# Optimization experiments

Hardware: AMD Instinct MI355X
Metric: run time of the kernel (lower is better)

Reference implementation:

```python
import jax, jax.numpy as jnp
import numpy as np

N_HEADS = 16
LOCAL_WINDOW = 512
MAX_REL_DIST = 128
NEG_INF = jnp.float32(-1e30)


def setup_inputs() -> dict:
    key = jax.random.key(0)
    ks = jax.random.split(key, 5)
    B, T, C = 2, 2048, 1024
    x = jax.random.normal(ks[0], (B, T, C), dtype=jnp.float32)
    w_qkv = jax.random.normal(ks[1], (3 * C, C), dtype=jnp.float32) * 0.02
    w_proj = jax.random.normal(ks[2], (C, C), dtype=jnp.float32) * 0.02
    b_proj = jax.random.normal(ks[3], (C,), dtype=jnp.float32) * 0.02
    rel_bias = jax.random.normal(ks[4], (2 * MAX_REL_DIST + 1, N_HEADS), dtype=jnp.float32) * 0.02
    return {"x": x, "w_qkv": w_qkv, "w_proj": w_proj, "b_proj": b_proj, "rel_bias": rel_bias}


def reference(x, w_qkv, w_proj, b_proj, rel_bias):
    B, T, C = x.shape
    H = N_HEADS
    hd = C // H
    scale = hd ** -0.5
    # qkv projection: (B,T,3C) -> (3,B,H,T,hd)
    qkv = (x @ w_qkv.T).reshape(B, T, 3, H, hd).transpose(2, 0, 3, 1, 4)
    q, k, v = qkv[0], qkv[1], qkv[2]
    # full TxT scores (faithful to eager original)
    attn = jnp.einsum('bhqd,bhkd->bhqk', q, k) * scale
    i = jnp.arange(T)[:, None]
    j = jnp.arange(T)[None, :]
    mask = (i >= j) & (jnp.abs(i - j) <= LOCAL_WINDOW)
    attn = jnp.where(mask[None, None], attn, NEG_INF)
    # relative position bias: (H,T,T)
    rel = jnp.clip(i - j, -MAX_REL_DIST, MAX_REL_DIST) + MAX_REL_DIST
    bias = rel_bias[rel].transpose(2, 0, 1)  # (H,T,T)
    attn = attn + bias[None]
    attn = jax.nn.softmax(attn, axis=-1)
    y = jnp.einsum('bhqk,bhkd->bhqd', attn, v)
    y = y.transpose(0, 2, 1, 3).reshape(B, T, C)
    y = y @ w_proj.T + b_proj
    return y
```

## Files before the change

kernel.cpp:

```cpp
#include <hip/hip_runtime.h>

#define T_SEQ 2048
#define HD 64

typedef float f32x4 __attribute__((ext_vector_type(4)));
typedef __bf16 bf16x8 __attribute__((ext_vector_type(8)));
typedef unsigned short ushort4v __attribute__((ext_vector_type(4)));
typedef unsigned short ushort8v __attribute__((ext_vector_type(8)));

__device__ __forceinline__ unsigned short f2bf(float f) {
    unsigned u = __builtin_bit_cast(unsigned, f);
    u += 0x7fffu + ((u >> 16) & 1u);
    return (unsigned short)(u >> 16);
}

__device__ __forceinline__ void gll16(const void* g, void* lds) {
    __builtin_amdgcn_global_load_lds(
        (const __attribute__((address_space(1))) unsigned int*)g,
        (__attribute__((address_space(3))) unsigned int*)lds, 16, 0, 0);
}

__device__ __forceinline__ bf16x8 ldfrag(const unsigned short* p) {
    return __builtin_bit_cast(bf16x8, *reinterpret_cast<const ushort8v*>(p));
}

__global__ __launch_bounds__(256)
void cvt_all_kernel(const float* __restrict__ x, const float* __restrict__ wq,
                    const float* __restrict__ wp, unsigned short* __restrict__ xb,
                    unsigned short* __restrict__ wqb, unsigned short* __restrict__ wpb)
{
    int bid = blockIdx.x;
    const float* s; unsigned short* d; int off;
    if (bid < 2048)      { s = x;  d = xb;  off = bid; }
    else if (bid < 3584) { s = wq; d = wqb; off = bid - 2048; }
    else                 { s = wp; d = wpb; off = bid - 3584; }
    int i = (off * 256 + threadIdx.x) * 8;
    f32x4 a = *reinterpret_cast<const f32x4*>(s + i);
    f32x4 b = *reinterpret_cast<const f32x4*>(s + i + 4);
    ushort8v o;
#pragma unroll
    for (int j = 0; j < 4; ++j) { o[j] = f2bf(a[j]); o[4 + j] = f2bf(b[j]); }
    *reinterpret_cast<ushort8v*>(d + i) = o;
}

__global__ __launch_bounds__(512, 6)
void gemm_qkv_kernel(const unsigned short* __restrict__ A, const unsigned short* __restrict__ W,
                     unsigned short* __restrict__ qo, unsigned short* __restrict__ ko,
                     unsigned short* __restrict__ vo)
{
    constexpr int K = 1024;
    __shared__ unsigned short As[128 * 32];
    __shared__ unsigned short Bs[128 * 32];
    const int t = threadIdx.x;
    const int m0 = blockIdx.x * 128, n0 = blockIdx.y * 128;
    const int lane = t & 63, w = t >> 6;
    const int wy = w >> 1, wx = w & 1;
    const int l15 = lane & 15, quad = lane >> 4;

    f32x4 acc[2][4] = {};
    const char* Ab = (const char*)A;
    const char* Wb = (const char*)W;

    const int srow = w * 16 + (lane >> 2);
    const int slot = (lane & 3) ^ ((lane >> 2) & 3);

    for (int kcl = 0; kcl < K; kcl += 32) {
        gll16(Ab + ((size_t)(n0 + srow) * K + kcl + slot * 8) * 2, (char*)As + w * 1024);
        gll16(Wb + ((size_t)(m0 + srow) * K + kcl + slot * 8) * 2, (char*)Bs + w * 1024);
        __syncthreads();
        bf16x8 af[2], bfr[4];
#pragma unroll
        for (int nt = 0; nt < 2; ++nt)
            af[nt] = ldfrag(As + (wy * 32 + nt * 16 + l15) * 32 + ((quad ^ (l15 & 3)) * 8));
#pragma unroll
        for (int mt = 0; mt < 4; ++mt)
            bfr[mt] = ldfrag(Bs + (wx * 64 + mt * 16 + l15) * 32 + ((quad ^ (l15 & 3)) * 8));
#pragma unroll
        for (int nt = 0; nt < 2; ++nt)
#pragma unroll
            for (int mt = 0; mt < 4; ++mt)
                acc[nt][mt] = __builtin_amdgcn_mfma_f32_16x16x32_bf16(af[nt], bfr[mt], acc[nt][mt], 0, 0, 0);
        __syncthreads();
    }

    const int s = m0 >> 10;
#pragma unroll
    for (int nt = 0; nt < 2; ++nt) {
#pragma unroll
        for (int mt = 0; mt < 4; ++mt) {
            const int m = m0 + wx * 64 + mt * 16 + l15;
            const int h = (m >> 6) & 15, d = m & 63;
#pragma unroll
            for (int r = 0; r < 4; ++r) {
                const int n = n0 + wy * 32 + nt * 16 + quad * 4 + r;
                const int bb = n >> 11, tt = n & 2047;
                float val = acc[nt][mt][r];
                if (s == 0)
                    qo[((size_t)((bb << 4) + h) * T_SEQ + tt) * HD + d] = f2bf(val * 0.125f);
                else if (s == 1)
                    ko[((size_t)((bb << 4) + h) * T_SEQ + tt) * HD + d] = f2bf(val);
                else
                    vo[((size_t)((bb << 4) + h) * HD + d) * T_SEQ + tt] = f2bf(val);
            }
        }
    }
}

__global__ __launch_bounds__(256)
void gemm_proj_kernel(const unsigned short* __restrict__ A, const unsigned short* __restrict__ W,
                      float* __restrict__ o0, const float* __restrict__ bias)
{
    constexpr int K = 1024;
    __shared__ unsigned short As[64 * 32];
    __shared__ unsigned short Bs[64 * 32];
    const int t = threadIdx.x;
    const int m0 = blockIdx.x * 64, n0 = blockIdx.y * 64;
    const int lane = t & 63, w = t >> 6;
    const int wy = w >> 1, wx = w & 1;
    const int l15 = lane & 15, quad = lane >> 4;

    f32x4 acc[2][2] = {};
    const char* Ab = (const char*)A;
    const char* Wb = (const char*)W;
    const int srow = t >> 2;
    const int skc = (t & 3) ^ (srow & 3);

    for (int kcl = 0; kcl < K; kcl += 32) {
        gll16(Ab + ((size_t)(n0 + srow) * K + kcl + skc * 8) * 2, (char*)As + w * 1024);
        gll16(Wb + ((size_t)(m0 + srow) * K + kcl + skc * 8) * 2, (char*)Bs + w * 1024);
        __syncthreads();
        bf16x8 af[2], bfr[2];
#pragma unroll
        for (int nt = 0; nt < 2; ++nt)
            af[nt] = ldfrag(As + (wy * 32 + nt * 16 + l15) * 32 + ((quad ^ (l15 & 3)) * 8));
#pragma unroll
        for (int mt = 0; mt < 2; ++mt)
            bfr[mt] = ldfrag(Bs + (wx * 32 + mt * 16 + l15) * 32 + ((quad ^ (l15 & 3)) * 8));
#pragma unroll
        for (int nt = 0; nt < 2; ++nt)
#pragma unroll
            for (int mt = 0; mt < 2; ++mt)
                acc[nt][mt] = __builtin_amdgcn_mfma_f32_16x16x32_bf16(af[nt], bfr[mt], acc[nt][mt], 0, 0, 0);
        __syncthreads();
    }

#pragma unroll
    for (int nt = 0; nt < 2; ++nt)
#pragma unroll
        for (int mt = 0; mt < 2; ++mt) {
            const int m = m0 + wx * 32 + mt * 16 + l15;
            const float bm = bias[m];
#pragma unroll
            for (int r = 0; r < 4; ++r) {
                const int n = n0 + wy * 32 + nt * 16 + quad * 4 + r;
                o0[(size_t)n * 1024 + m] = acc[nt][mt][r] + bm;
            }
        }
}

__global__ __launch_bounds__(512, 4)
void attn_kernel(const unsigned short* __restrict__ qg, const unsigned short* __restrict__ kg,
                 const unsigned short* __restrict__ vt, const float* __restrict__ rel_bias,
                 unsigned short* __restrict__ y)
{
    __shared__ unsigned short Ks[64 * 64];
    __shared__ unsigned short Vt[64 * 64];
    __shared__ unsigned short Pl[8 * 16 * 72];
    __shared__ float bias_s[260];

    const int t = threadIdx.x;
    const int lane = t & 63, w = t >> 6;
    const int l15 = lane & 15, quad = lane >> 4;
    const int flat = blockIdx.x;
    const int xcd = flat & 7, within = flat >> 3;
    const int bh = xcd * 4 + (within >> 4);
    const int qt = within & 15;
    const int b = bh >> 4, h = bh & 15;
    const int q0 = qt << 7;
    const int qw0 = q0 + w * 16;
    const int q_row = qw0 + l15;
    const size_t base = (size_t)bh * T_SEQ * HD;

    for (int i = t; i < 257; i += 512) bias_s[i] = rel_bias[i * 16 + h];

    bf16x8 qf[2];
#pragma unroll
    for (int ks = 0; ks < 2; ++ks)
        qf[ks] = ldfrag(qg + base + (size_t)q_row * HD + ks * 32 + quad * 8);

    float m_r = -1e30f, l_r = 0.f;
    f32x4 Oacc[4] = {};

    unsigned short* Pme = Pl + w * (16 * 72);
    const int srow = t >> 3;
    const int skc = (t & 7) ^ (srow & 7);

    const int kt0 = (qt * 2 > 8) ? (qt * 2 - 8) : 0;
    const int kt1 = qt * 2 + 1;

    for (int kt = kt0; kt <= kt1; ++kt) {
        gll16((const char*)(kg + base + (size_t)(kt * 64 + srow) * HD + skc * 8), (char*)Ks + w * 1024);
        gll16((const char*)(vt + base + (size_t)srow * T_SEQ + kt * 64 + skc * 8), (char*)Vt + w * 1024);
        __syncthreads();

        const int delta = qw0 - kt * 64;
        if (delta >= 0 && delta <= 560) {
            f32x4 Sacc[4] = {};
#pragma unroll
            for (int ks = 0; ks < 2; ++ks)
#pragma unroll
                for (int ct = 0; ct < 4; ++ct) {
                    bf16x8 kf = ldfrag(Ks + (ct * 16 + l15) * 64 + (((ks * 4 + quad) ^ (l15 & 7)) * 8));
                    Sacc[ct] = __builtin_amdgcn_mfma_f32_16x16x32_bf16(kf, qf[ks], Sacc[ct], 0, 0, 0);
                }

            float sv[4][4];
            if (delta >= 192 && delta <= 496) {
                const float bC = bias_s[256];
#pragma unroll
                for (int ct = 0; ct < 4; ++ct)
#pragma unroll
                    for (int r = 0; r < 4; ++r) sv[ct][r] = Sacc[ct][r] + bC;
            } else {
#pragma unroll
                for (int ct = 0; ct < 4; ++ct)
#pragma unroll
                    for (int r = 0; r < 4; ++r) {
                        int diff = q_row - (kt * 64 + ct * 16 + quad * 4 + r);
                        float bb = bias_s[(diff < 128 ? diff : 128) + 128];
                        float s = Sacc[ct][r] + bb;
                        sv[ct][r] = (diff < 0 || diff > 512) ? -1e30f : s;
                    }
            }

            float mx = -1e30f;
#pragma unroll
            for (int ct = 0; ct < 4; ++ct)
#pragma unroll
                for (int r = 0; r < 4; ++r) mx = fmaxf(mx, sv[ct][r]);
            mx = fmaxf(mx, __shfl_xor(mx, 16, 64));
            mx = fmaxf(mx, __shfl_xor(mx, 32, 64));
            float mn = fmaxf(m_r, mx);
            float alpha = __expf(m_r - mn);
            m_r = mn;
            float ps = 0.f;
            float p[4][4];
#pragma unroll
            for (int ct = 0; ct < 4; ++ct)
#pragma unroll
                for (int r = 0; r < 4; ++r) { p[ct][r] = __expf(sv[ct][r] - mn); ps += p[ct][r]; }
            ps += __shfl_xor(ps, 16, 64);
            ps += __shfl_xor(ps, 32, 64);
            l_r = l_r * alpha + ps;

#pragma unroll
            for (int ct = 0; ct < 4; ++ct) {
                ushort4v pw;
#pragma unroll
                for (int j = 0; j < 4; ++j) pw[j] = f2bf(p[ct][j]);
                *reinterpret_cast<ushort4v*>(Pme + l15 * 72 + ct * 16 + quad * 4) = pw;
            }
#pragma unroll
            for (int mt = 0; mt < 4; ++mt) Oacc[mt] *= alpha;
#pragma unroll
            for (int ks = 0; ks < 2; ++ks) {
                bf16x8 pf = ldfrag(Pme + l15 * 72 + ks * 32 + quad * 8);
#pragma unroll
                for (int mt = 0; mt < 4; ++mt) {
                    bf16x8 vf = ldfrag(Vt + (mt * 16 + l15) * 64 + (((ks * 4 + quad) ^ (l15 & 7)) * 8));
                    Oacc[mt] = __builtin_amdgcn_mfma_f32_16x16x32_bf16(vf, pf, Oacc[mt], 0, 0, 0);
                }
            }
        }
        __syncthreads();
    }

    const float inv = 1.0f / l_r;
    unsigned short* yp = y + ((size_t)b * T_SEQ + q_row) * 1024 + h * 64;
#pragma unroll
    for (int mt = 0; mt < 4; ++mt) {
        ushort4v o;
#pragma unroll
        for (int j = 0; j < 4; ++j) o[j] = f2bf(Oacc[mt][j] * inv);
        *reinterpret_cast<ushort4v*>(yp + mt * 16 + quad * 4) = o;
    }
}

extern "C" void kernel_launch(void* const* d_in, const int* in_sizes, int n_in,
                              void* d_out, int out_size, void* d_ws, size_t ws_size,
                              hipStream_t stream)
{
    (void)in_sizes; (void)n_in; (void)out_size; (void)ws_size;
    const float* x        = (const float*)d_in[0];
    const float* w_qkv    = (const float*)d_in[1];
    const float* w_proj   = (const float*)d_in[2];
    const float* b_proj   = (const float*)d_in[3];
    const float* rel_bias = (const float*)d_in[4];
    float* out = (float*)d_out;

    unsigned short* ws = (unsigned short*)d_ws;
    unsigned short* xb     = ws;
    unsigned short* wqkvb  = xb + 4194304;
    unsigned short* wprojb = wqkvb + 3145728;
    unsigned short* qb     = wprojb + 1048576;
    unsigned short* kb     = qb + 4194304;
    unsigned short* vtb    = kb + 4194304;
    unsigned short* yab    = vtb + 4194304;

    cvt_all_kernel<<<4096, 256, 0, stream>>>(x, w_qkv, w_proj, xb, wqkvb, wprojb);
    gemm_qkv_kernel<<<dim3(24, 32), 512, 0, stream>>>(xb, wqkvb, qb, kb, vtb);
    attn_kernel<<<512, 512, 0, stream>>>(qb, kb, vtb, rel_bias, yab);
    gemm_proj_kernel<<<dim3(16, 64), 256, 0, stream>>>(yab, wprojb, out, b_proj);
}
```

Baseline: 169.3 us.

## Deepen GEMM K-tiles to 64 and enlarge projection GEMM tile to 128x64

Result: slower. 182.3 us (+7.7%).

```diff
diff --git a/kernel.cpp b/kernel.cpp
--- a/kernel.cpp
+++ b/kernel.cpp
@@ -49,8 +49,8 @@
                      unsigned short* __restrict__ vo)
 {
     constexpr int K = 1024;
-    __shared__ unsigned short As[128 * 32];
-    __shared__ unsigned short Bs[128 * 32];
+    __shared__ unsigned short As[128 * 64];
+    __shared__ unsigned short Bs[128 * 64];
     const int t = threadIdx.x;
     const int m0 = blockIdx.x * 128, n0 = blockIdx.y * 128;
     const int lane = t & 63, w = t >> 6;
@@ -61,25 +61,37 @@
     const char* Ab = (const char*)A;
     const char* Wb = (const char*)W;
 
-    const int srow = w * 16 + (lane >> 2);
-    const int slot = (lane & 3) ^ ((lane >> 2) & 3);
-
-    for (int kcl = 0; kcl < K; kcl += 32) {
-        gll16(Ab + ((size_t)(n0 + srow) * K + kcl + slot * 8) * 2, (char*)As + w * 1024);
-        gll16(Wb + ((size_t)(m0 + srow) * K + kcl + slot * 8) * 2, (char*)Bs + w * 1024);
-        __syncthreads();
-        bf16x8 af[2], bfr[4];
-#pragma unroll
-        for (int nt = 0; nt < 2; ++nt)
-            af[nt] = ldfrag(As + (wy * 32 + nt * 16 + l15) * 32 + ((quad ^ (l15 & 3)) * 8));
-#pragma unroll
-        for (int mt = 0; mt < 4; ++mt)
-            bfr[mt] = ldfrag(Bs + (wx * 64 + mt * 16 + l15) * 32 + ((quad ^ (l15 & 3)) * 8));
-#pragma unroll
-        for (int nt = 0; nt < 2; ++nt)
-#pragma unroll
-            for (int mt = 0; mt < 4; ++mt)
-                acc[nt][mt] = __builtin_amdgcn_mfma_f32_16x16x32_bf16(af[nt], bfr[mt], acc[nt][mt], 0, 0, 0);
+    const int lrow = lane >> 3;
+    const int gslot = (lane & 7) ^ lrow;
+
+    for (int kcl = 0; kcl < K; kcl += 64) {
+#pragma unroll
+        for (int i = 0; i < 2; ++i) {
+            int c = w * 2 + i;
+            int row = c * 8 + lrow;
+            gll16(Ab + (((size_t)(n0 + row) * K + kcl + gslot * 8) * 2), (char*)As + c * 1024);
+            gll16(Wb + (((size_t)(m0 + row) * K + kcl + gslot * 8) * 2), (char*)Bs + c * 1024);
+        }
+        __syncthreads();
+#pragma unroll
+        for (int ks = 0; ks < 2; ++ks) {
+            bf16x8 af[2], bfr[4];
+#pragma unroll
+            for (int nt = 0; nt < 2; ++nt) {
+                int row = wy * 32 + nt * 16 + l15;
+                af[nt] = ldfrag(As + row * 64 + (((ks * 4 + quad) ^ (row & 7)) * 8));
+            }
+#pragma unroll
+            for (int mt = 0; mt < 4; ++mt) {
+                int row = wx * 64 + mt * 16 + l15;
+                bfr[mt] = ldfrag(Bs + row * 64 + (((ks * 4 + quad) ^ (row & 7)) * 8));
+            }
+#pragma unroll
+            for (int nt = 0; nt < 2; ++nt)
+#pragma unroll
+                for (int mt = 0; mt < 4; ++mt)
+                    acc[nt][mt] = __builtin_amdgcn_mfma_f32_16x16x32_bf16(af[nt], bfr[mt], acc[nt][mt], 0, 0, 0);
+        }
         __syncthreads();
     }
 
@@ -111,48 +123,65 @@
                       float* __restrict__ o0, const float* __restrict__ bias)
 {
     constexpr int K = 1024;
-    __shared__ unsigned short As[64 * 32];
-    __shared__ unsigned short Bs[64 * 32];
+    __shared__ unsigned short As[128 * 64];
+    __shared__ unsigned short Bs[64 * 64];
     const int t = threadIdx.x;
-    const int m0 = blockIdx.x * 64, n0 = blockIdx.y * 64;
+    const int m0 = blockIdx.x * 64, n0 = blockIdx.y * 128;
     const int lane = t & 63, w = t >> 6;
     const int wy = w >> 1, wx = w & 1;
     const int l15 = lane & 15, quad = lane >> 4;
 
-    f32x4 acc[2][2] = {};
+    f32x4 acc[4][2] = {};
     const char* Ab = (const char*)A;
     const char* Wb = (const char*)W;
-    const int srow = t >> 2;
-    const int skc = (t & 3) ^ (srow & 3);
-
-    for (int kcl = 0; kcl < K; kcl += 32) {
-        gll16(Ab + ((size_t)(n0 + srow) * K + kcl + skc * 8) * 2, (char*)As + w * 1024);
-        gll16(Wb + ((size_t)(m0 + srow) * K + kcl + skc * 8) * 2, (char*)Bs + w * 1024);
-        __syncthreads();
-        bf16x8 af[2], bfr[2];
-#pragma unroll
-        for (int nt = 0; nt < 2; ++nt)
-            af[nt] = ldfrag(As + (wy * 32 + nt * 16 + l15) * 32 + ((quad ^ (l15 & 3)) * 8));
-#pragma unroll
-        for (int mt = 0; mt < 2; ++mt)
-            bfr[mt] = ldfrag(Bs + (wx * 32 + mt * 16 + l15) * 32 + ((quad ^ (l15 & 3)) * 8));
-#pragma unroll
-        for (int nt = 0; nt < 2; ++nt)
-#pragma unroll
-            for (int mt = 0; mt < 2; ++mt)
-                acc[nt][mt] = __builtin_amdgcn_mfma_f32_16x16x32_bf16(af[nt], bfr[mt], acc[nt][mt], 0, 0, 0);
-        __syncthreads();
-    }
-
-#pragma unroll
-    for (int nt = 0; nt < 2; ++nt)
+    const int lrow = lane >> 3;
+    const int gslot = (lane & 7) ^ lrow;
+
+    for (int kcl = 0; kcl < K; kcl += 64) {
+#pragma unroll
+        for (int i = 0; i < 4; ++i) {
+            int c = w * 4 + i;
+            int row = c * 8 + lrow;
+            gll16(Ab + (((size_t)(n0 + row) * K + kcl + gslot * 8) * 2), (char*)As + c * 1024);
+        }
+#pragma unroll
+        for (int i = 0; i < 2; ++i) {
+            int c = w * 2 + i;
+            int row = c * 8 + lrow;
+            gll16(Wb + (((size_t)(m0 + row) * K + kcl + gslot * 8) * 2), (char*)Bs + c * 1024);
+        }
+        __syncthreads();
+#pragma unroll
+        for (int ks = 0; ks < 2; ++ks) {
+            bf16x8 af[4], bfr[2];
+#pragma unroll
+            for (int nt = 0; nt < 4; ++nt) {
+                int row = wy * 64 + nt * 16 + l15;
+                af[nt] = ldfrag(As + row * 64 + (((ks * 4 + quad) ^ (row & 7)) * 8));
+            }
+#pragma unroll
+            for (int mt = 0; mt < 2; ++mt) {
+                int row = wx * 32 + mt * 16 + l15;
+                bfr[mt] = ldfrag(Bs + row * 64 + (((ks * 4 + quad) ^ (row & 7)) * 8));
+            }
+#pragma unroll
+            for (int nt = 0; nt < 4; ++nt)
+#pragma unroll
+                for (int mt = 0; mt < 2; ++mt)
+                    acc[nt][mt] = __builtin_amdgcn_mfma_f32_16x16x32_bf16(af[nt], bfr[mt], acc[nt][mt], 0, 0, 0);
+        }
+        __syncthreads();
+    }
+
+#pragma unroll
+    for (int nt = 0; nt < 4; ++nt)
 #pragma unroll
         for (int mt = 0; mt < 2; ++mt) {
             const int m = m0 + wx * 32 + mt * 16 + l15;
             const float bm = bias[m];
 #pragma unroll
             for (int r = 0; r < 4; ++r) {
-                const int n = n0 + wy * 32 + nt * 16 + quad * 4 + r;
+                const int n = n0 + wy * 64 + nt * 16 + quad * 4 + r;
                 o0[(size_t)n * 1024 + m] = acc[nt][mt][r] + bm;
             }
         }
@@ -310,5 +339,5 @@
     cvt_all_kernel<<<4096, 256, 0, stream>>>(x, w_qkv, w_proj, xb, wqkvb, wprojb);
     gemm_qkv_kernel<<<dim3(24, 32), 512, 0, stream>>>(xb, wqkvb, qb, kb, vtb);
     attn_kernel<<<512, 512, 0, stream>>>(qb, kb, vtb, rel_bias, yab);
-    gemm_proj_kernel<<<dim3(16, 64), 256, 0, stream>>>(yab, wprojb, out, b_proj);
-}
+    gemm_proj_kernel<<<dim3(16, 32), 256, 0, stream>>>(yab, wprojb, out, b_proj);
+}
```

## Give each attention wave two 16-row query tiles and halve the block size

Applied to the files above, without the earlier changes.

Measured after the change: 176.7 us. 1.04x slower.

```diff
diff --git a/kernel.cpp b/kernel.cpp
--- a/kernel.cpp
+++ b/kernel.cpp
@@ -158,14 +158,14 @@
         }
 }
 
-__global__ __launch_bounds__(512, 4)
+__global__ __launch_bounds__(256)
 void attn_kernel(const unsigned short* __restrict__ qg, const unsigned short* __restrict__ kg,
                  const unsigned short* __restrict__ vt, const float* __restrict__ rel_bias,
                  unsigned short* __restrict__ y)
 {
     __shared__ unsigned short Ks[64 * 64];
     __shared__ unsigned short Vt[64 * 64];
-    __shared__ unsigned short Pl[8 * 16 * 72];
+    __shared__ unsigned short Pl[4 * 2 * 16 * 72];
     __shared__ float bias_s[260];
 
     const int t = threadIdx.x;
@@ -177,113 +177,136 @@
     const int qt = within & 15;
     const int b = bh >> 4, h = bh & 15;
     const int q0 = qt << 7;
-    const int qw0 = q0 + w * 16;
-    const int q_row = qw0 + l15;
+    const int qw0 = q0 + w * 32;
     const size_t base = (size_t)bh * T_SEQ * HD;
 
-    for (int i = t; i < 257; i += 512) bias_s[i] = rel_bias[i * 16 + h];
-
-    bf16x8 qf[2];
-#pragma unroll
-    for (int ks = 0; ks < 2; ++ks)
-        qf[ks] = ldfrag(qg + base + (size_t)q_row * HD + ks * 32 + quad * 8);
-
-    float m_r = -1e30f, l_r = 0.f;
-    f32x4 Oacc[4] = {};
-
-    unsigned short* Pme = Pl + w * (16 * 72);
+    for (int i = t; i < 257; i += 256) bias_s[i] = rel_bias[i * 16 + h];
+
+    bf16x8 qf[2][2];
+#pragma unroll
+    for (int qq = 0; qq < 2; ++qq)
+#pragma unroll
+        for (int ks = 0; ks < 2; ++ks)
+            qf[qq][ks] = ldfrag(qg + base + (size_t)(qw0 + qq * 16 + l15) * HD + ks * 32 + quad * 8);
+
+    float m_r[2] = {-1e30f, -1e30f}, l_r[2] = {0.f, 0.f};
+    f32x4 Oacc[2][4] = {};
+
+    unsigned short* Pme = Pl + w * (2 * 16 * 72);
     const int srow = t >> 3;
-    const int skc = (t & 7) ^ (srow & 7);
 
     const int kt0 = (qt * 2 > 8) ? (qt * 2 - 8) : 0;
     const int kt1 = qt * 2 + 1;
 
     for (int kt = kt0; kt <= kt1; ++kt) {
-        gll16((const char*)(kg + base + (size_t)(kt * 64 + srow) * HD + skc * 8), (char*)Ks + w * 1024);
-        gll16((const char*)(vt + base + (size_t)srow * T_SEQ + kt * 64 + skc * 8), (char*)Vt + w * 1024);
+#pragma unroll
+        for (int i = 0; i < 2; ++i) {
+            int g = t + i * 256;
+            int sr = g >> 3;
+            int sk = (g & 7) ^ (sr & 7);
+            gll16((const char*)(kg + base + (size_t)(kt * 64 + sr) * HD + sk * 8),
+                  (char*)Ks + i * 4096 + w * 1024);
+            gll16((const char*)(vt + base + (size_t)sr * T_SEQ + kt * 64 + sk * 8),
+                  (char*)Vt + i * 4096 + w * 1024);
+        }
         __syncthreads();
 
         const int delta = qw0 - kt * 64;
-        if (delta >= 0 && delta <= 560) {
-            f32x4 Sacc[4] = {};
+        if (delta >= 0 && delta <= 544) {
+            f32x4 Sacc[2][4] = {};
 #pragma unroll
             for (int ks = 0; ks < 2; ++ks)
 #pragma unroll
                 for (int ct = 0; ct < 4; ++ct) {
                     bf16x8 kf = ldfrag(Ks + (ct * 16 + l15) * 64 + (((ks * 4 + quad) ^ (l15 & 7)) * 8));
-                    Sacc[ct] = __builtin_amdgcn_mfma_f32_16x16x32_bf16(kf, qf[ks], Sacc[ct], 0, 0, 0);
+#pragma unroll
+                    for (int qq = 0; qq < 2; ++qq)
+                        Sacc[qq][ct] = __builtin_amdgcn_mfma_f32_16x16x32_bf16(kf, qf[qq][ks], Sacc[qq][ct], 0, 0, 0);
                 }
 
-            float sv[4][4];
-            if (delta >= 192 && delta <= 496) {
-                const float bC = bias_s[256];
+            const bool fast = (delta >= 192 && delta <= 480);
+            const float bC = bias_s[256];
+#pragma unroll
+            for (int qq = 0; qq < 2; ++qq) {
+                const int q_row = qw0 + qq * 16 + l15;
+                float sv[4][4];
+                if (fast) {
+#pragma unroll
+                    for (int ct = 0; ct < 4; ++ct)
+#pragma unroll
+                        for (int r = 0; r < 4; ++r) sv[ct][r] = Sacc[qq][ct][r] + bC;
+                } else {
+#pragma unroll
+                    for (int ct = 0; ct < 4; ++ct)
+#pragma unroll
+                        for (int r = 0; r < 4; ++r) {
+                            int diff = q_row - (kt * 64 + ct * 16 + quad * 4 + r);
+                            float bb2 = bias_s[(diff < 128 ? diff : 128) + 128];
+                            float sx = Sacc[qq][ct][r] + bb2;
+                            sv[ct][r] = (diff < 0 || diff > 512) ? -1e30f : sx;
+                        }
+                }
+
+                float mx = -1e30f;
 #pragma unroll
                 for (int ct = 0; ct < 4; ++ct)
 #pragma unroll
-                    for (int r = 0; r < 4; ++r) sv[ct][r] = Sacc[ct][r] + bC;
-            } else {
-#pragma unroll
-                for (int ct = 0; ct < 4; ++ct)
+                    for (int r = 0; r < 4; ++r) mx = fmaxf(mx, sv[ct][r]);
+                mx = fmaxf(mx, __shfl_xor(mx, 16, 64));
+                mx = fmaxf(mx, __shfl_xor(mx, 32, 64));
+                float mn = fmaxf(m_r[qq], mx);
+                float alpha = __expf(m_r[qq] - mn);
+                m_r[qq] = mn;
+                float ps = 0.f;
+#pragma unroll
+                for (int ct = 0; ct < 4; ++ct) {
+                    ushort4v pw;
 #pragma unroll
                     for (int r = 0; r < 4; ++r) {
-                        int diff = q_row - (kt * 64 + ct * 16 + quad * 4 + r);
-                        float bb = bias_s[(diff < 128 ? diff : 128) + 128];
-                        float s = Sacc[ct][r] + bb;
-                        sv[ct][r] = (diff < 0 || diff > 512) ? -1e30f : s;
+                        float p = __expf(sv[ct][r] - mn);
+                        ps += p;
+                        pw[r] = f2bf(p);
                     }
+                    *reinterpret_cast<ushort4v*>(Pme + qq * (16 * 72) + l15 * 72 + ct * 16 + quad * 4) = pw;
+                }
+                ps += __shfl_xor(ps, 16, 64);
+                ps += __shfl_xor(ps, 32, 64);
+                l_r[qq] = l_r[qq] * alpha + ps;
+#pragma unroll
+                for (int mt = 0; mt < 4; ++mt) Oacc[qq][mt] *= alpha;
             }
 
-            float mx = -1e30f;
-#pragma unroll
-            for (int ct = 0; ct < 4; ++ct)
-#pragma unroll
-                for (int r = 0; r < 4; ++r) mx = fmaxf(mx, sv[ct][r]);
-            mx = fmaxf(mx, __shfl_xor(mx, 16, 64));
-            mx = fmaxf(mx, __shfl_xor(mx, 32, 64));
-            float mn = fmaxf(m_r, mx);
-            float alpha = __expf(m_r - mn);
-            m_r = mn;
-            float ps = 0.f;
-            float p[4][4];
-#pragma unroll
-            for (int ct = 0; ct < 4; ++ct)
-#pragma unroll
-                for (int r = 0; r < 4; ++r) { p[ct][r] = __expf(sv[ct][r] - mn); ps += p[ct][r]; }
-            ps += __shfl_xor(ps, 16, 64);
-            ps += __shfl_xor(ps, 32, 64);
-            l_r = l_r * alpha + ps;
-
-#pragma unroll
-            for (int ct = 0; ct < 4; ++ct) {
-                ushort4v pw;
-#pragma unroll
-                for (int j = 0; j < 4; ++j) pw[j] = f2bf(p[ct][j]);
-                *reinterpret_cast<ushort4v*>(Pme + l15 * 72 + ct * 16 + quad * 4) = pw;
-            }
-#pragma unroll
-            for (int mt = 0; mt < 4; ++mt) Oacc[mt] *= alpha;
 #pragma unroll
             for (int ks = 0; ks < 2; ++ks) {
-                bf16x8 pf = ldfrag(Pme + l15 * 72 + ks * 32 + quad * 8);
+                bf16x8 pf[2];
+#pragma unroll
+                for (int qq = 0; qq < 2; ++qq)
+                    pf[qq] = ldfrag(Pme + qq * (16 * 72) + l15 * 72 + ks * 32 + quad * 8);
 #pragma unroll
                 for (int mt = 0; mt < 4; ++mt) {
                     bf16x8 vf = ldfrag(Vt + (mt * 16 + l15) * 64 + (((ks * 4 + quad) ^ (l15 & 7)) * 8));
-                    Oacc[mt] = __builtin_amdgcn_mfma_f32_16x16x32_bf16(vf, pf, Oacc[mt], 0, 0, 0);
+#pragma unroll
+                    for (int qq = 0; qq < 2; ++qq)
+                        Oacc[qq][mt] = __builtin_amdgcn_mfma_f32_16x16x32_bf16(vf, pf[qq], Oacc[qq][mt], 0, 0, 0);
                 }
             }
         }
         __syncthreads();
     }
 
-    const float inv = 1.0f / l_r;
-    unsigned short* yp = y + ((size_t)b * T_SEQ + q_row) * 1024 + h * 64;
-#pragma unroll
-    for (int mt = 0; mt < 4; ++mt) {
-        ushort4v o;
-#pragma unroll
-        for (int j = 0; j < 4; ++j) o[j] = f2bf(Oacc[mt][j] * inv);
-        *reinterpret_cast<ushort4v*>(yp + mt * 16 + quad * 4) = o;
-    }
+#pragma unroll
+    for (int qq = 0; qq < 2; ++qq) {
+        const float inv = 1.0f / l_r[qq];
+        unsigned short* yp = y + ((size_t)b * T_SEQ + qw0 + qq * 16 + l15) * 1024 + h * 64;
+#pragma unroll
+        for (int mt = 0; mt < 4; ++mt) {
+            ushort4v o;
+#pragma unroll
+            for (int j = 0; j < 4; ++j) o[j] = f2bf(Oacc[qq][mt][j] * inv);
+            *reinterpret_cast<ushort4v*>(yp + mt * 16 + quad * 4) = o;
+        }
+    }
+    (void)srow;
 }
 
 extern "C" void kernel_launch(void* const* d_in, const int* in_sizes, int n_in,
@@ -309,6 +332,6 @@
 
     cvt_all_kernel<<<4096, 256, 0, stream>>>(x, w_qkv, w_proj, xb, wqkvb, wprojb);
     gemm_qkv_kernel<<<dim3(24, 32), 512, 0, stream>>>(xb, wqkvb, qb, kb, vtb);
-    attn_kernel<<<512, 512, 0, stream>>>(qb, kb, vtb, rel_bias, yab);
+    attn_kernel<<<512, 256, 0, stream>>>(qb, kb, vtb, rel_bias, yab);
     gemm_proj_kernel<<<dim3(16, 64), 256, 0, stream>>>(yab, wprojb, out, b_proj);
 }
```
